# Optimization experiments

Measured on AMD Instinct MI355X. Metric: run time of the kernel, lower is better.

The kernel has to match this reference:

```python
import jax, jax.numpy as jnp
import numpy as np

B, T, D, H = 64, 512, 256, 1024
INIT_S = 0.005


def setup_inputs() -> dict:
    key = jax.random.key(0)
    ks = jax.random.split(key, 8)
    gate_bias = float(np.log(INIT_S / (1.0 - INIT_S)))
    # Linear weights in torch layout [out, in]; y = x @ W.T + b.
    # Gate weights (Ws, Us) are zero-init in the module; we use small random
    # values so the gate path actually exercises the math.
    return {
        "x": jax.random.normal(ks[0], (B, T, D), dtype=jnp.float32),
        "Wx_w": jax.random.normal(ks[1], (H, D), dtype=jnp.float32) / np.sqrt(D),
        "Wx_b": jnp.zeros((H,), dtype=jnp.float32),
        "Wh_w": jax.random.normal(ks[2], (H, H), dtype=jnp.float32) / np.sqrt(H),
        "Ws_w": jax.random.normal(ks[3], (1, D), dtype=jnp.float32) * 0.01,
        "Ws_b": jnp.full((1,), gate_bias, dtype=jnp.float32),
        "Us_w": jax.random.normal(ks[4], (1, H), dtype=jnp.float32) * 0.01,
        "out_w": jax.random.normal(ks[5], (1, H), dtype=jnp.float32) / np.sqrt(H),
        "out_b": jnp.zeros((1,), dtype=jnp.float32),
    }


def reference(x, Wx_w, Wx_b, Wh_w, Ws_w, Ws_b, Us_w, out_w, out_b):
    # SharedGateRNN.forward_with_intermediates (ln=False, gate_rescale=None)
    wh_diag = jnp.diagonal(Wh_w)        # [H]
    us_vec = Us_w.reshape(-1)           # [H]

    def step(h_prev, x_t):
        # x_t: [B, D], h_prev: [B, H]
        a_s = x_t @ Ws_w.T + Ws_b + h_prev @ Us_w.T     # [B, 1]
        s = jax.nn.sigmoid(a_s)                          # [B, 1] scalar gate
        pre = x_t @ Wx_w.T + Wx_b + h_prev @ Wh_w.T      # [B, H]
        h_tilde = jnp.tanh(pre)
        h = (1.0 - s) * h_prev + s * h_tilde             # broadcast gate over H
        y = h @ out_w.T + out_b                          # [B, 1]
        gate_s = jnp.broadcast_to(s, h.shape)
        leak = 1.0 - gate_s
        tanh_prime = 1.0 - h_tilde ** 2
        s_prime = s * (1.0 - s)                          # [B, 1]
        rdiag = (h_tilde - h_prev) * (s_prime * us_vec) + s * tanh_prime * wh_diag
        return h, (y, h, gate_s, leak, rdiag)

    h0 = jnp.zeros((x.shape[0], H), dtype=x.dtype)
    x_t_first = jnp.transpose(x, (1, 0, 2))              # [T, B, D]
    _, (ys, hs, gates, leaks, rdiags) = jax.lax.scan(step, h0, x_t_first)

    swap = lambda a: jnp.transpose(a, (1, 0, 2))         # [T,B,*] -> [B,T,*]
    return (swap(ys), swap(hs), swap(gates), swap(leaks), swap(rdiags))
```

## Files before the change

### kernel.cpp

```cpp
#include <hip/hip_runtime.h>

#define NT 512
#define ND 256
#define NH 1024
#define NB 64

typedef float f32x4 __attribute__((ext_vector_type(4)));
typedef short bf16x8 __attribute__((ext_vector_type(8)));

__device__ __forceinline__ unsigned short f2bf(float f) {
  unsigned u = __builtin_bit_cast(unsigned, f);
  u += 0x7fffu + ((u >> 16) & 1u);
  return (unsigned short)(u >> 16);
}
__device__ __forceinline__ float bflo(unsigned u) {
  return __builtin_bit_cast(float, u << 16);
}
__device__ __forceinline__ float bfhi(unsigned u) {
  return __builtin_bit_cast(float, u & 0xffff0000u);
}
__device__ __forceinline__ bf16x8 pack8(float4 a, float4 b) {
  bf16x8 r;
  r[0] = (short)f2bf(a.x); r[1] = (short)f2bf(a.y);
  r[2] = (short)f2bf(a.z); r[3] = (short)f2bf(a.w);
  r[4] = (short)f2bf(b.x); r[5] = (short)f2bf(b.y);
  r[6] = (short)f2bf(b.z); r[7] = (short)f2bf(b.w);
  return r;
}

__global__ void __launch_bounds__(256, 1)
rnn_step_kernel(const float* __restrict__ x,
                const float* __restrict__ Wx_w,
                const float* __restrict__ Wx_b,
                const float* __restrict__ Wh_w,
                const float* __restrict__ Ws_w,
                const float* __restrict__ Ws_b,
                const float* __restrict__ Us_w,
                float* __restrict__ out,
                unsigned short* __restrict__ hbuf,
                unsigned int* __restrict__ flags)
{
  const int tid = (int)threadIdx.x;
  const int w   = tid >> 6;
  const int l   = tid & 63;
  const int bm  = l & 15;
  const int lg  = l >> 4;
  const int sl  = (int)blockIdx.x & 63;
  const int bg  = (int)blockIdx.x >> 6;
  const int r_base = sl * 16;
  const int b_base = bg * 16;
  const int ro = tid & 15;
  const int bo = tid >> 4;
  const int rg = r_base + ro;
  const int b_glob = b_base + bo;

  __shared__ unsigned short us_sh[1024];
  __shared__ float cpart[4][4][72];
  __shared__ float gpart[4][16];

  {
    const float4 uv = *(const float4*)(Us_w + tid*4);
    us_sh[tid*4+0] = f2bf(uv.x); us_sh[tid*4+1] = f2bf(uv.y);
    us_sh[tid*4+2] = f2bf(uv.z); us_sh[tid*4+3] = f2bf(uv.w);
  }

  bf16x8 whf[8];
  bf16x8 wxf[2];
  float4 wsf[4];
  {
    const int ar = r_base + bm;
    #pragma unroll
    for (int m = 0; m < 8; ++m) {
      const int k0 = w*256 + m*32 + lg*8;
      const float4 f0 = *(const float4*)(Wh_w + (size_t)ar*NH + k0);
      const float4 f1 = *(const float4*)(Wh_w + (size_t)ar*NH + k0 + 4);
      whf[m] = pack8(f0, f1);
    }
    #pragma unroll
    for (int m = 0; m < 2; ++m) {
      const int k0 = w*64 + m*32 + lg*8;
      const float4 f0 = *(const float4*)(Wx_w + (size_t)ar*ND + k0);
      const float4 f1 = *(const float4*)(Wx_w + (size_t)ar*ND + k0 + 4);
      wxf[m] = pack8(f0, f1);
      wsf[m*2]   = *(const float4*)(Ws_w + k0);
      wsf[m*2+1] = *(const float4*)(Ws_w + k0 + 4);
    }
  }
  const float wxb_r = Wx_b[rg];
  const float whd_r = Wh_w[(size_t)rg*NH + rg];
  const float usr_r = Us_w[rg];
  const float wsb   = Ws_b[0];

  float* const hs_o = out + (size_t)NB*NT;
  float* const g_o  = hs_o + (size_t)NB*NT*NH;
  float* const l_o  = g_o  + (size_t)NB*NT*NH;
  float* const rd_o = l_o  + (size_t)NB*NT*NH;

  __syncthreads();

  float myh = 0.f;

  for (int t = 0; t < NT; ++t) {
    f32x4 acc = {0.f, 0.f, 0.f, 0.f};
    float ga = 0.f;
    {
      const float* xrow = x + ((size_t)(b_base+bm)*NT + t)*ND + w*64 + lg*8;
      #pragma unroll
      for (int m = 0; m < 2; ++m) {
        const float4 f0 = *(const float4*)(xrow + m*32);
        const float4 f1 = *(const float4*)(xrow + m*32 + 4);
        acc = __builtin_amdgcn_mfma_f32_16x16x32_bf16(
                wxf[m], pack8(f0, f1), acc, 0, 0, 0);
        ga += wsf[m*2].x*f0.x + wsf[m*2].y*f0.y + wsf[m*2].z*f0.z + wsf[m*2].w*f0.w
            + wsf[m*2+1].x*f1.x + wsf[m*2+1].y*f1.y + wsf[m*2+1].z*f1.z + wsf[m*2+1].w*f1.w;
      }
    }

    if (t > 0) {
      {
        const unsigned int* fp = flags + ((size_t)bg*NT + (t-1))*64 + l;
        while (true) {
          unsigned int v;
          asm volatile("global_load_dword %0, %1, off sc0 sc1\n\t"
                       "s_waitcnt vmcnt(0)"
                       : "=v"(v) : "v"(fp) : "memory");
          if (__all((int)(v != 0u))) break;
          __builtin_amdgcn_s_sleep(1);
        }
      }
      const unsigned short* hrow =
          hbuf + ((size_t)((t-1)&1)*NB + b_base + bm)*NH + w*256 + lg*8;
      uint4 hv[8];
      #pragma unroll
      for (int m = 0; m < 8; ++m)
        asm volatile("global_load_dwordx4 %0, %1, off sc0 sc1"
                     : "=v"(hv[m]) : "v"(hrow + m*32) : "memory");
      asm volatile("s_waitcnt vmcnt(0)" ::: "memory");
      __builtin_amdgcn_sched_barrier(0);
      #pragma unroll
      for (int m = 0; m < 8; ++m) {
        acc = __builtin_amdgcn_mfma_f32_16x16x32_bf16(
                whf[m], __builtin_bit_cast(bf16x8, hv[m]), acc, 0, 0, 0);
        const uint4 uu = *(const uint4*)&us_sh[w*256 + m*32 + lg*8];
        ga += bflo(uu.x)*bflo(hv[m].x) + bfhi(uu.x)*bfhi(hv[m].x)
            + bflo(uu.y)*bflo(hv[m].y) + bfhi(uu.y)*bfhi(hv[m].y)
            + bflo(uu.z)*bflo(hv[m].z) + bfhi(uu.z)*bfhi(hv[m].z)
            + bflo(uu.w)*bflo(hv[m].w) + bfhi(uu.w)*bfhi(hv[m].w);
      }
    }

    ga += __shfl_xor(ga, 16, 64);
    ga += __shfl_xor(ga, 32, 64);
    if (l < 16) gpart[w][l] = ga;
    cpart[w][0][l] = acc[0];
    cpart[w][1][l] = acc[1];
    cpart[w][2][l] = acc[2];
    cpart[w][3][l] = acc[3];
    __syncthreads();

    const float gsum = gpart[0][bo] + gpart[1][bo] + gpart[2][bo] + gpart[3][bo];
    const int ci = ro & 3, cl = ((ro >> 2) << 4) + bo;
    const float pre0 = cpart[0][ci][cl] + cpart[1][ci][cl] +
                       cpart[2][ci][cl] + cpart[3][ci][cl];
    const float sg   = 1.f / (1.f + expf(-(gsum + wsb)));
    const float pre  = pre0 + wxb_r;
    const float htld = tanhf(pre);
    const float hp   = myh;
    const float h    = (1.f - sg)*hp + sg*htld;
    myh = h;
    {
      const unsigned hb = (unsigned)f2bf(h);
      unsigned short* hptr = hbuf + ((size_t)(t & 1)*NB + b_glob)*NH + rg;
      asm volatile("global_store_short %0, %1, off sc0 sc1"
                   :: "v"(hptr), "v"(hb) : "memory");
    }
    asm volatile("s_waitcnt vmcnt(0)" ::: "memory");
    __syncthreads();
    if (tid == 0) {
      unsigned int one = 1u;
      unsigned int* fp = flags + ((size_t)bg*NT + t)*64 + sl;
      asm volatile("global_store_dword %0, %1, off sc0 sc1"
                   :: "v"(fp), "v"(one) : "memory");
    }

    {
      const size_t obase = ((size_t)b_glob*NT + t)*NH + rg;
      const float sp = sg * (1.f - sg);
      __builtin_nontemporal_store(h, &hs_o[obase]);
      __builtin_nontemporal_store(sg, &g_o[obase]);
      __builtin_nontemporal_store(1.f - sg, &l_o[obase]);
      __builtin_nontemporal_store((htld - hp)*(sp*usr_r) + sg*(1.f - htld*htld)*whd_r,
                                  &rd_o[obase]);
    }
  }
}

__global__ void yfinish_kernel(const float* __restrict__ hs,
                               const float* __restrict__ out_w,
                               const float* __restrict__ out_b,
                               float* __restrict__ ys)
{
  const int row  = (int)blockIdx.x*4 + ((int)threadIdx.x >> 6);
  const int lane = (int)threadIdx.x & 63;
  const float4* hp = (const float4*)(hs + (size_t)row*NH);
  const float4* wp = (const float4*)out_w;
  float s = 0.f;
  #pragma unroll
  for (int i = 0; i < 4; ++i) {
    const float4 h4 = hp[i*64 + lane];
    const float4 w4 = wp[i*64 + lane];
    s += h4.x*w4.x + h4.y*w4.y + h4.z*w4.z + h4.w*w4.w;
  }
  #pragma unroll
  for (int off = 32; off > 0; off >>= 1) s += __shfl_xor(s, off, 64);
  if (lane == 0) ys[row] = s + out_b[0];
}

extern "C" void kernel_launch(void* const* d_in, const int* in_sizes, int n_in,
                              void* d_out, int out_size, void* d_ws, size_t ws_size,
                              hipStream_t stream)
{
  (void)in_sizes; (void)n_in; (void)out_size; (void)ws_size;
  const float* x     = (const float*)d_in[0];
  const float* Wx_w  = (const float*)d_in[1];
  const float* Wx_b  = (const float*)d_in[2];
  const float* Wh_w  = (const float*)d_in[3];
  const float* Ws_w  = (const float*)d_in[4];
  const float* Ws_b  = (const float*)d_in[5];
  const float* Us_w  = (const float*)d_in[6];
  const float* out_w = (const float*)d_in[7];
  const float* out_b = (const float*)d_in[8];
  float* out = (float*)d_out;

  char* ws = (char*)d_ws;
  unsigned short* hbuf = (unsigned short*)ws;
  unsigned int* flags  = (unsigned int*)(ws + 262144);

  hipMemsetAsync(flags, 0, (size_t)4*NT*64*sizeof(unsigned int), stream);
  rnn_step_kernel<<<dim3(256), dim3(256), 0, stream>>>(
      x, Wx_w, Wx_b, Wh_w, Ws_w, Ws_b, Us_w, out, hbuf, flags);
  yfinish_kernel<<<dim3((NB*NT)/4), dim3(256), 0, stream>>>(
      out + (size_t)NB*NT, out_w, out_b, out);
}
```

Measured before the change: 1.834 ms.

## Replace flag-based step sync with tagged hidden-state words polled directly

Each hidden-state value is now stored as a 32-bit word that packs the bf16 value with a 16-bit timestep tag. Consumers poll the h rows themselves until every tag matches, which removes the separate flag array, the store-wait, the extra block barrier and the flag write. The shared-memory partial buffers are double-buffered so the dropped barrier does not cause a race. In exchange each poll reads twice as many bytes, and the hidden-state buffer must be zeroed before launch.

```diff
diff --git a/kernel.cpp b/kernel.cpp
--- a/kernel.cpp
+++ b/kernel.cpp
@@ -37,8 +37,7 @@
                 const float* __restrict__ Ws_b,
                 const float* __restrict__ Us_w,
                 float* __restrict__ out,
-                unsigned short* __restrict__ hbuf,
-                unsigned int* __restrict__ flags)
+                unsigned* __restrict__ hbuf)
 {
   const int tid = (int)threadIdx.x;
   const int w   = tid >> 6;
@@ -55,8 +54,8 @@
   const int b_glob = b_base + bo;
 
   __shared__ unsigned short us_sh[1024];
-  __shared__ float cpart[4][4][72];
-  __shared__ float gpart[4][16];
+  __shared__ float cpart[2][4][4][72];
+  __shared__ float gpart[2][4][16];
 
   {
     const float4 uv = *(const float4*)(Us_w + tid*4);
@@ -101,6 +100,7 @@
   float myh = 0.f;
 
   for (int t = 0; t < NT; ++t) {
+    const int p = t & 1;
     f32x4 acc = {0.f, 0.f, 0.f, 0.f};
     float ga = 0.f;
     {
@@ -117,51 +117,59 @@
     }
 
     if (t > 0) {
-      {
-        const unsigned int* fp = flags + ((size_t)bg*NT + (t-1))*64 + l;
-        while (true) {
-          unsigned int v;
-          asm volatile("global_load_dword %0, %1, off sc0 sc1\n\t"
-                       "s_waitcnt vmcnt(0)"
-                       : "=v"(v) : "v"(fp) : "memory");
-          if (__all((int)(v != 0u))) break;
-          __builtin_amdgcn_s_sleep(1);
-        }
+      const unsigned tag = (unsigned)t & 0xffffu;
+      const unsigned* hrow =
+          hbuf + ((size_t)((t-1)&1)*NB + b_base + bm)*NH + w*256 + lg*8;
+      uint4 hv[16];
+      while (true) {
+        #pragma unroll
+        for (int m = 0; m < 8; ++m)
+          asm volatile("global_load_dwordx4 %0, %2, off sc0 sc1\n\t"
+                       "global_load_dwordx4 %1, %2, off offset:16 sc0 sc1"
+                       : "=&v"(hv[2*m]), "=&v"(hv[2*m+1])
+                       : "v"(hrow + (size_t)m*32) : "memory");
+        asm volatile("s_waitcnt vmcnt(0)" ::: "memory");
+        bool ok = true;
+        #pragma unroll
+        for (int i = 0; i < 16; ++i)
+          ok = ok & ((hv[i].x & 0xffffu) == tag) & ((hv[i].y & 0xffffu) == tag)
+                  & ((hv[i].z & 0xffffu) == tag) & ((hv[i].w & 0xffffu) == tag);
+        if (__all((int)ok)) break;
+        __builtin_amdgcn_s_sleep(1);
       }
-      const unsigned short* hrow =
-          hbuf + ((size_t)((t-1)&1)*NB + b_base + bm)*NH + w*256 + lg*8;
-      uint4 hv[8];
-      #pragma unroll
-      for (int m = 0; m < 8; ++m)
-        asm volatile("global_load_dwordx4 %0, %1, off sc0 sc1"
-                     : "=v"(hv[m]) : "v"(hrow + m*32) : "memory");
-      asm volatile("s_waitcnt vmcnt(0)" ::: "memory");
       __builtin_amdgcn_sched_barrier(0);
       #pragma unroll
       for (int m = 0; m < 8; ++m) {
+        const uint4 a0 = hv[2*m], a1 = hv[2*m+1];
+        uint4 bu;
+        bu.x = (a0.x >> 16) | (a0.y & 0xffff0000u);
+        bu.y = (a0.z >> 16) | (a0.w & 0xffff0000u);
+        bu.z = (a1.x >> 16) | (a1.y & 0xffff0000u);
+        bu.w = (a1.z >> 16) | (a1.w & 0xffff0000u);
         acc = __builtin_amdgcn_mfma_f32_16x16x32_bf16(
-                whf[m], __builtin_bit_cast(bf16x8, hv[m]), acc, 0, 0, 0);
+                whf[m], __builtin_bit_cast(bf16x8, bu), acc, 0, 0, 0);
         const uint4 uu = *(const uint4*)&us_sh[w*256 + m*32 + lg*8];
-        ga += bflo(uu.x)*bflo(hv[m].x) + bfhi(uu.x)*bfhi(hv[m].x)
-            + bflo(uu.y)*bflo(hv[m].y) + bfhi(uu.y)*bfhi(hv[m].y)
-            + bflo(uu.z)*bflo(hv[m].z) + bfhi(uu.z)*bfhi(hv[m].z)
-            + bflo(uu.w)*bflo(hv[m].w) + bfhi(uu.w)*bfhi(hv[m].w);
+        ga += bflo(uu.x)*bfhi(a0.x) + bfhi(uu.x)*bfhi(a0.y)
+            + bflo(uu.y)*bfhi(a0.z) + bfhi(uu.y)*bfhi(a0.w)
+            + bflo(uu.z)*bfhi(a1.x) + bfhi(uu.z)*bfhi(a1.y)
+            + bflo(uu.w)*bfhi(a1.z) + bfhi(uu.w)*bfhi(a1.w);
       }
     }
 
     ga += __shfl_xor(ga, 16, 64);
     ga += __shfl_xor(ga, 32, 64);
-    if (l < 16) gpart[w][l] = ga;
-    cpart[w][0][l] = acc[0];
-    cpart[w][1][l] = acc[1];
-    cpart[w][2][l] = acc[2];
-    cpart[w][3][l] = acc[3];
+    if (l < 16) gpart[p][w][l] = ga;
+    cpart[p][w][0][l] = acc[0];
+    cpart[p][w][1][l] = acc[1];
+    cpart[p][w][2][l] = acc[2];
+    cpart[p][w][3][l] = acc[3];
     __syncthreads();
 
-    const float gsum = gpart[0][bo] + gpart[1][bo] + gpart[2][bo] + gpart[3][bo];
+    const float gsum = gpart[p][0][bo] + gpart[p][1][bo] +
+                       gpart[p][2][bo] + gpart[p][3][bo];
     const int ci = ro & 3, cl = ((ro >> 2) << 4) + bo;
-    const float pre0 = cpart[0][ci][cl] + cpart[1][ci][cl] +
-                       cpart[2][ci][cl] + cpart[3][ci][cl];
+    const float pre0 = cpart[p][0][ci][cl] + cpart[p][1][ci][cl] +
+                       cpart[p][2][ci][cl] + cpart[p][3][ci][cl];
     const float sg   = 1.f / (1.f + expf(-(gsum + wsb)));
     const float pre  = pre0 + wxb_r;
     const float htld = tanhf(pre);
@@ -169,18 +177,10 @@
     const float h    = (1.f - sg)*hp + sg*htld;
     myh = h;
     {
-      const unsigned hb = (unsigned)f2bf(h);
-      unsigned short* hptr = hbuf + ((size_t)(t & 1)*NB + b_glob)*NH + rg;
-      asm volatile("global_store_short %0, %1, off sc0 sc1"
-                   :: "v"(hptr), "v"(hb) : "memory");
-    }
-    asm volatile("s_waitcnt vmcnt(0)" ::: "memory");
-    __syncthreads();
-    if (tid == 0) {
-      unsigned int one = 1u;
-      unsigned int* fp = flags + ((size_t)bg*NT + t)*64 + sl;
+      const unsigned word = ((unsigned)f2bf(h) << 16) | ((unsigned)(t+1) & 0xffffu);
+      unsigned* hptr = hbuf + ((size_t)p*NB + b_glob)*NH + rg;
       asm volatile("global_store_dword %0, %1, off sc0 sc1"
-                   :: "v"(fp), "v"(one) : "memory");
+                   :: "v"(hptr), "v"(word) : "memory");
     }
 
     {
@@ -232,13 +232,11 @@
   const float* out_b = (const float*)d_in[8];
   float* out = (float*)d_out;
 
-  char* ws = (char*)d_ws;
-  unsigned short* hbuf = (unsigned short*)ws;
-  unsigned int* flags  = (unsigned int*)(ws + 262144);
-
-  hipMemsetAsync(flags, 0, (size_t)4*NT*64*sizeof(unsigned int), stream);
+  unsigned* hbuf = (unsigned*)d_ws;
+
+  hipMemsetAsync(hbuf, 0, (size_t)2*NB*NH*sizeof(unsigned), stream);
   rnn_step_kernel<<<dim3(256), dim3(256), 0, stream>>>(
-      x, Wx_w, Wx_b, Wh_w, Ws_w, Ws_b, Us_w, out, hbuf, flags);
+      x, Wx_w, Wx_b, Wh_w, Ws_w, Ws_b, Us_w, out, hbuf);
   yfinish_kernel<<<dim3((NB*NT)/4), dim3(256), 0, stream>>>(
       out + (size_t)NB*NT, out_w, out_b, out);
 }
```

After: 2.375 ms. 1.29x slower.
